# Kernel optimization log

Measured on AMD Instinct MI355X. Metric: run time of the kernel, lower is better.

## Reference

```python
import jax, jax.numpy as jnp
import numpy as np

ALPHA = 0.2  # LeakyReLU negative slope
NEG_INF = -9e15


def _xavier(key, shape, gain=1.414):
    fan_in, fan_out = shape[-2], shape[-1]
    lim = gain * np.sqrt(6.0 / (fan_in + fan_out))
    return jax.random.uniform(key, shape, jnp.float32, -lim, lim)


def setup_inputs() -> dict:
    key = jax.random.key(0)
    ks = jax.random.split(key, 8)
    B, N, Din, H, Dh, Do = 8, 1024, 256, 4, 128, 64
    x = jax.random.normal(ks[0], (B, N, Din), jnp.float32)
    adj = jax.random.randint(ks[1], (B, N, N), 0, 2).astype(jnp.int32)
    W_heads = _xavier(ks[2], (H, Din, Dh))                 # per-head W
    a_heads = _xavier(ks[3], (H, 2 * Dh, 1))[..., 0]       # per-head a, [H, 2*Dh]
    W_out = _xavier(ks[4], (H * Dh, Do))                   # out_att W
    a_out = _xavier(ks[5], (2 * Do, 1))[..., 0]            # out_att a, [2*Do]
    Wf = _xavier(ks[6], (Do, Do), gain=1.0)                # fc_out linear
    bf = jnp.zeros((Do,), jnp.float32)
    return {"x": x, "adj": adj, "W_heads": W_heads, "a_heads": a_heads,
            "W_out": W_out, "a_out": a_out, "Wf": Wf, "bf": bf}


def _leaky_relu(v):
    return jnp.where(v >= 0, v, ALPHA * v)


def _gat(h, adj, W, a):
    # h: [B,N,Fin], adj: [B,N,N], W: [Fin,Fout], a: [2*Fout]
    Wh = h @ W                                   # [B,N,F]
    F = W.shape[-1]
    # additive attention: e_ij = leakyrelu(a_src.Wh_i + a_dst.Wh_j)
    src = Wh @ a[:F]                             # [B,N]
    dst = Wh @ a[F:]                             # [B,N]
    e = _leaky_relu(src[:, :, None] + dst[:, None, :])   # [B,N,N]
    scores = jnp.where(adj > 0, e, NEG_INF)
    attn = jax.nn.softmax(scores, axis=-1)       # dropout is a no-op in eval
    return attn @ Wh                             # [B,N,F]


def reference(x, adj, W_heads, a_heads, W_out, a_out, Wf, bf):
    B, N, _ = x.shape
    H, _, Dh = W_heads.shape
    # multi-head GAT, heads vmapped over leading axis of W_heads / a_heads
    heads = jax.vmap(_gat, in_axes=(None, None, 0, 0))(x, adj, W_heads, a_heads)  # [H,B,N,Dh]
    xcat = jnp.moveaxis(heads, 0, 2).reshape(B, N, H * Dh)   # concat heads, dim=2
    out = jax.nn.elu(_gat(xcat, adj, W_out, a_out))           # [B,N,Do]
    out = jax.nn.relu(out @ Wf + bf)                          # fc_out (dropout no-op)
    return out
```

## Files before the change

### kernel.cpp

```cpp
#include <hip/hip_runtime.h>
#include <hip/hip_bf16.h>

#define BSZ 8
#define NN 1024
#define DIN 256
#define NH 4
#define DH 128
#define DOUT 64
#define RTOT (BSZ*NN)
#define FCAT (NH*DH)
#define ALPHA 0.2f
#define XBLK 1024

typedef unsigned short ushortT;
typedef __attribute__((ext_vector_type(8))) short bf16x8;
typedef __attribute__((ext_vector_type(4))) float f32x4;

static __device__ __forceinline__ ushortT f2bf(float f) {
    __hip_bfloat16 h = __float2bfloat16(f);
    return *reinterpret_cast<ushortT*>(&h);
}
static __device__ __forceinline__ float bfu2f(ushortT u) {
    return __uint_as_float(((unsigned)u) << 16);
}
static __device__ __forceinline__ void split2(float v, ushortT& hi, ushortT& lo) {
    hi = f2bf(v);
    lo = f2bf(v - bfu2f(hi));
}
static __device__ __forceinline__ void gload16(const ushortT* g, ushortT* l) {
    __builtin_amdgcn_global_load_lds(
        (const __attribute__((address_space(1))) unsigned int*)(const void*)g,
        (__attribute__((address_space(3))) unsigned int*)(void*)l, 16, 0, 0);
}

__global__ __launch_bounds__(256) void k_prepw(const float* __restrict__ x,
                                               const float* __restrict__ W,
                                               const float* __restrict__ Wout,
                                               ushortT* __restrict__ xbh, ushortT* __restrict__ xbl,
                                               ushortT* __restrict__ WbTh, ushortT* __restrict__ WbTl,
                                               ushortT* __restrict__ WoTh, ushortT* __restrict__ WoTl) {
    const int bx = blockIdx.x;
    if (bx < XBLK) {
        const int g = bx * 256 + threadIdx.x;
        const float4* p = (const float4*)x + (size_t)g * 2;
        union { ushortT u[8]; uint4 q; } th, tl;
#pragma unroll
        for (int e4 = 0; e4 < 2; ++e4) {
            const float4 v = p[e4];
            split2(v.x, th.u[e4 * 4 + 0], tl.u[e4 * 4 + 0]);
            split2(v.y, th.u[e4 * 4 + 1], tl.u[e4 * 4 + 1]);
            split2(v.z, th.u[e4 * 4 + 2], tl.u[e4 * 4 + 2]);
            split2(v.w, th.u[e4 * 4 + 3], tl.u[e4 * 4 + 3]);
        }
        ((uint4*)xbh)[g] = th.q;
        ((uint4*)xbl)[g] = tl.q;
        return;
    }
    const int g2 = (bx - XBLK) * 256 + threadIdx.x;
    if (g2 < NH * DH * DIN) {
        const int h = g2 >> 15, f = (g2 >> 8) & 127, k = g2 & 255;
        const int kt = k >> 6, k64 = k & 63;
        const float v = W[(size_t)h * DIN * DH + (size_t)k * DH + f];
        ushortT hi, lo; split2(v, hi, lo);
        const int idx = ((h * 4 + kt) * 128 + f) * 64 + k64;
        WbTh[idx] = hi; WbTl[idx] = lo;
    } else {
        const int g3 = g2 - NH * DH * DIN;
        const int f = g3 >> 9, k = g3 & 511;
        const float v = Wout[(size_t)k * DOUT + f];
        ushortT hi, lo; split2(v, hi, lo);
        WoTh[g3] = hi; WoTl[g3] = lo;
    }
}

__global__ __launch_bounds__(512) void k_main(const ushortT* __restrict__ xbh,
                                              const ushortT* __restrict__ xbl,
                                              const float* __restrict__ ah_,
                                              const ushortT* __restrict__ WbTh,
                                              const ushortT* __restrict__ WbTl,
                                              const int* __restrict__ adj,
                                              unsigned* __restrict__ adjbit,
                                              ushortT* __restrict__ WhT,
                                              float* __restrict__ src1,
                                              float* __restrict__ dst1) {
    __shared__ ushortT Ah[128 * 64], Al[128 * 64];
    __shared__ ushortT Bh[128 * 64], Bl[128 * 64];
    __shared__ float sred[8][32], dred[8][32];
    const int tid = threadIdx.x;
    if (blockIdx.x >= 256) {
        const int g = (blockIdx.x - 256) * 512 + tid;
        const int row = g >> 5, w = g & 31;
        const int4* p = (const int4*)(adj + (size_t)row * NN + w * 32);
        unsigned m = 0;
#pragma unroll
        for (int q = 0; q < 8; ++q) {
            const int4 v = p[q];
            m |= (v.x > 0 ? 1u : 0u) << (q * 4 + 0);
            m |= (v.y > 0 ? 1u : 0u) << (q * 4 + 1);
            m |= (v.z > 0 ? 1u : 0u) << (q * 4 + 2);
            m |= (v.w > 0 ? 1u : 0u) << (q * 4 + 3);
        }
        adjbit[g] = m;
        return;
    }
    const int lane = tid & 63, wave = tid >> 6;
    const int h = blockIdx.x >> 6, mt = blockIdx.x & 63;
    const int r0 = mt * 128, b = r0 >> 10, jr = r0 & 1023;
    const int m16 = lane & 15, quad = lane >> 4;
    const int mg = wave >> 1, fg = wave & 1;
    f32x4 acc[2][4];
#pragma unroll
    for (int a = 0; a < 2; ++a)
#pragma unroll
        for (int c = 0; c < 4; ++c) acc[a][c] = (f32x4){0.f, 0.f, 0.f, 0.f};

    for (int kt = 0; kt < 4; ++kt) {
        __syncthreads();
        const ushortT* planeH = WbTh + (size_t)((h * 4 + kt) * 128) * 64;
        const ushortT* planeL = WbTl + (size_t)((h * 4 + kt) * 128) * 64;
#pragma unroll
        for (int half = 0; half < 2; ++half) {
            const int f = wave * 16 + half * 8 + (lane >> 3);
            const int sc = (lane & 7) ^ (f & 7);
            gload16(planeH + (size_t)f * 64 + sc * 8, Bh + (wave * 16 + half * 8) * 64);
            gload16(planeL + (size_t)f * 64 + sc * 8, Bl + (wave * 16 + half * 8) * 64);
        }
#pragma unroll
        for (int half = 0; half < 2; ++half) {
            const int r = wave * 16 + half * 8 + (lane >> 3);
            const int sc = (lane & 7) ^ (r & 7);
            gload16(xbh + (size_t)(r0 + r) * DIN + kt * 64 + sc * 8, Ah + (wave * 16 + half * 8) * 64);
            gload16(xbl + (size_t)(r0 + r) * DIN + kt * 64 + sc * 8, Al + (wave * 16 + half * 8) * 64);
        }
        __syncthreads();
#pragma unroll
        for (int ks = 0; ks < 2; ++ks) {
            bf16x8 a_h[2], a_l[2], b_h[4], b_l[4];
#pragma unroll
            for (int ms = 0; ms < 2; ++ms) {
                const int row = (mg * 2 + ms) * 16 + m16;
                const int cl = (ks * 4 + quad) ^ (row & 7);
                a_h[ms] = *(const bf16x8*)&Ah[row * 64 + cl * 8];
                a_l[ms] = *(const bf16x8*)&Al[row * 64 + cl * 8];
            }
#pragma unroll
            for (int fs = 0; fs < 4; ++fs) {
                const int row = (fg * 4 + fs) * 16 + m16;
                const int cl = (ks * 4 + quad) ^ (row & 7);
                b_h[fs] = *(const bf16x8*)&Bh[row * 64 + cl * 8];
                b_l[fs] = *(const bf16x8*)&Bl[row * 64 + cl * 8];
            }
#pragma unroll
            for (int ms = 0; ms < 2; ++ms)
#pragma unroll
                for (int fs = 0; fs < 4; ++fs) {
                    acc[ms][fs] = __builtin_amdgcn_mfma_f32_16x16x32_bf16(a_h[ms], b_h[fs], acc[ms][fs], 0, 0, 0);
                    acc[ms][fs] = __builtin_amdgcn_mfma_f32_16x16x32_bf16(a_h[ms], b_l[fs], acc[ms][fs], 0, 0, 0);
                    acc[ms][fs] = __builtin_amdgcn_mfma_f32_16x16x32_bf16(a_l[ms], b_h[fs], acc[ms][fs], 0, 0, 0);
                }
        }
    }
    float sacc[2][4] = {{0,0,0,0},{0,0,0,0}}, dacc[2][4] = {{0,0,0,0},{0,0,0,0}};
#pragma unroll
    for (int ms = 0; ms < 2; ++ms)
#pragma unroll
        for (int fs = 0; fs < 4; ++fs) {
            const int fl = (fg * 4 + fs) * 16 + m16;
            const float a_s = ah_[h * 2 * DH + fl];
            const float a_d = ah_[h * 2 * DH + DH + fl];
            union { ushortT u[4]; uint2 q; } tw;
#pragma unroll
            for (int reg = 0; reg < 4; ++reg) {
                const float v = acc[ms][fs][reg];
                sacc[ms][reg] += v * a_s;
                dacc[ms][reg] += v * a_d;
                tw.u[reg] = f2bf(v);
            }
            *(uint2*)(WhT + ((size_t)((b * NH + h) * DH + fl)) * NN + jr + (mg * 2 + ms) * 16 + quad * 4) = tw.q;
        }
#pragma unroll
    for (int ms = 0; ms < 2; ++ms) {
#pragma unroll
        for (int reg = 0; reg < 4; ++reg) {
            float s = sacc[ms][reg], d = dacc[ms][reg];
#pragma unroll
            for (int o = 8; o > 0; o >>= 1) {
                s += __shfl_xor(s, o, 64);
                d += __shfl_xor(d, o, 64);
            }
            if (m16 == 0) {
                sred[wave][ms * 16 + quad * 4 + reg] = s;
                dred[wave][ms * 16 + quad * 4 + reg] = d;
            }
        }
    }
    __syncthreads();
    if (tid < 128) {
        const int mgr = tid >> 5, idx = tid & 31;
        src1[h * RTOT + r0 + tid] = sred[mgr * 2][idx] + sred[mgr * 2 + 1][idx];
        dst1[h * RTOT + r0 + tid] = dred[mgr * 2][idx] + dred[mgr * 2 + 1][idx];
    }
}

__global__ __launch_bounds__(512) void k_attn1(const unsigned* __restrict__ adjbit,
                                               const ushortT* __restrict__ WhT,
                                               const float* __restrict__ src1,
                                               const float* __restrict__ dst1,
                                               ushortT* __restrict__ xcat) {
    __shared__ ushortT As[2][64 * 64];
    __shared__ unsigned maskS[64 * 32];
    __shared__ float dstv[NN];
    __shared__ float srcv[64], rowinv[64], red8[8];
    const int tid = threadIdx.x, lane = tid & 63, wave = tid >> 6;
    const int bh = blockIdx.x & 31, it = blockIdx.x >> 5;
    const int b = bh >> 2, h = bh & 3;
    const int i0 = it * 64;
    const int m16 = lane & 15, quad = lane >> 4;
    const int mg = wave >> 2, fg = wave & 3;

    const unsigned* mbase = adjbit + (size_t)(b * NN + i0) * 32;
#pragma unroll
    for (int k2 = 0; k2 < 4; ++k2) maskS[tid + 512 * k2] = mbase[tid + 512 * k2];
    float lm = -INFINITY;
#pragma unroll
    for (int k2 = 0; k2 < 2; ++k2) {
        const float d = dst1[h * RTOT + b * NN + tid + 512 * k2];
        dstv[tid + 512 * k2] = d;
        lm = fmaxf(lm, d);
    }
    if (tid < 64) srcv[tid] = src1[h * RTOT + b * NN + i0 + tid];
#pragma unroll
    for (int o = 32; o > 0; o >>= 1) lm = fmaxf(lm, __shfl_xor(lm, o, 64));
    if (lane == 0) red8[wave] = lm;
    __syncthreads();
    float dmax = red8[0];
#pragma unroll
    for (int w = 1; w < 8; ++w) dmax = fmaxf(dmax, red8[w]);

    const int arow = tid >> 3, apart = tid & 7;
    const float si = srcv[arow];
    float mrow = si + dmax;
    mrow = mrow >= 0.f ? mrow : ALPHA * mrow;
    float fsum = 0.f;

    const ushortT* Bbase = WhT + (size_t)(bh * DH) * NN;
    f32x4 acc[2][2];
#pragma unroll
    for (int a = 0; a < 2; ++a)
#pragma unroll
        for (int c = 0; c < 2; ++c) acc[a][c] = (f32x4){0.f, 0.f, 0.f, 0.f};

#define STAGE_A(kt_, buf_)                                                                 \
    {                                                                                      \
        const int kt__ = (kt_);                                                            \
        const unsigned w0 = maskS[arow * 32 + kt__ * 2 + (apart >> 2)];                    \
        const int bb = (apart & 3) * 8;                                                    \
        union { ushortT u[8]; uint4 q; } tw;                                               \
        _Pragma("unroll")                                                                  \
        for (int e4 = 0; e4 < 2; ++e4) {                                                   \
            const float4 dv = *(const float4*)&dstv[kt__ * 64 + apart * 8 + e4 * 4];       \
            const float vv[4] = {dv.x, dv.y, dv.z, dv.w};                                  \
            _Pragma("unroll")                                                              \
            for (int e = 0; e < 4; ++e) {                                                  \
                float v = si + vv[e];                                                      \
                v = v >= 0.f ? v : ALPHA * v;                                              \
                const unsigned bit = (w0 >> (bb + e4 * 4 + e)) & 1u;                       \
                const float p = bit ? __expf(v - mrow) : 0.f;                              \
                fsum += p;                                                                 \
                tw.u[e4 * 4 + e] = f2bf(p);                                                \
            }                                                                              \
        }                                                                                  \
        *(uint4*)&As[(buf_)][arow * 64 + (apart ^ (arow & 7)) * 8] = tw.q;                 \
    }
#define LOADB(kt_, dst_)                                                                   \
    {                                                                                      \
        _Pragma("unroll")                                                                  \
        for (int ks = 0; ks < 2; ++ks)                                                     \
            _Pragma("unroll")                                                              \
            for (int ff = 0; ff < 2; ++ff)                                                 \
                dst_[ks][ff] = *(const bf16x8*)(Bbase +                                    \
                    (size_t)(fg * 32 + ff * 16 + m16) * NN + (kt_) * 64 + (ks * 4 + quad) * 8); \
    }
#define MFMA_STEP(buf_, bv_)                                                               \
    {                                                                                      \
        _Pragma("unroll")                                                                  \
        for (int ks = 0; ks < 2; ++ks) {                                                   \
            bf16x8 afr[2];                                                                 \
            _Pragma("unroll")                                                              \
            for (int ms = 0; ms < 2; ++ms) {                                               \
                const int rowa = mg * 32 + ms * 16 + m16;                                  \
                const int cla = (ks * 4 + quad) ^ (rowa & 7);                              \
                afr[ms] = *(const bf16x8*)&As[(buf_)][rowa * 64 + cla * 8];                \
            }                                                                              \
            _Pragma("unroll")                                                              \
            for (int ff = 0; ff < 2; ++ff)                                                 \
                _Pragma("unroll")                                                          \
                for (int ms = 0; ms < 2; ++ms)                                             \
                    acc[ms][ff] = __builtin_amdgcn_mfma_f32_16x16x32_bf16(afr[ms], bv_[ks][ff], acc[ms][ff], 0, 0, 0); \
        }                                                                                  \
    }

    bf16x8 b0v[2][2], b1v[2][2];
    LOADB(0, b0v);
    STAGE_A(0, 0);
    for (int kt = 0; kt < 16; kt += 2) {
        __syncthreads();
        if (kt < 15) { LOADB(kt + 1, b1v); STAGE_A(kt + 1, 1); }
        MFMA_STEP(0, b0v);
        __syncthreads();
        if (kt < 14) { LOADB(kt + 2, b0v); STAGE_A(kt + 2, 0); }
        MFMA_STEP(1, b1v);
    }
#undef STAGE_A
#undef LOADB
#undef MFMA_STEP
#pragma unroll
    for (int o = 1; o < 8; o <<= 1) fsum += __shfl_xor(fsum, o, 64);
    if ((lane & 7) == 0) rowinv[arow] = 1.f / fsum;
    __syncthreads();
#pragma unroll
    for (int ms = 0; ms < 2; ++ms) {
        float rv[4];
#pragma unroll
        for (int reg = 0; reg < 4; ++reg) rv[reg] = rowinv[mg * 32 + ms * 16 + quad * 4 + reg];
#pragma unroll
        for (int ff = 0; ff < 2; ++ff) {
            const int f = h * DH + fg * 32 + ff * 16 + m16;
#pragma unroll
            for (int reg = 0; reg < 4; ++reg) {
                const int i = i0 + mg * 32 + ms * 16 + quad * 4 + reg;
                xcat[(size_t)(b * NN + i) * FCAT + f] = f2bf(acc[ms][ff][reg] * rv[reg]);
            }
        }
    }
}

__global__ __launch_bounds__(256) void k_wh2(const ushortT* __restrict__ xcat,
                                             const ushortT* __restrict__ WoTh,
                                             const ushortT* __restrict__ WoTl,
                                             const float* __restrict__ aout,
                                             ushortT* __restrict__ Wh2T,
                                             float* __restrict__ src2,
                                             float* __restrict__ dst2) {
    __shared__ ushortT As[32 * 64];
    __shared__ ushortT Bh[64 * 64], Bl[64 * 64];
    __shared__ float sred[4][16], dred[4][16];
    const int tid = threadIdx.x, lane = tid & 63, wave = tid >> 6;
    const int r0 = blockIdx.x * 32;
    const int b = r0 >> 10, jr = r0 & 1023;
    const int m16 = lane & 15, quad = lane >> 4;
    const int mg = wave >> 1, fg = wave & 1;
    f32x4 acc[2] = {(f32x4){0.f,0.f,0.f,0.f}, (f32x4){0.f,0.f,0.f,0.f}};

    for (int kt = 0; kt < 8; ++kt) {
        __syncthreads();
        {
            const int row = wave * 8 + (lane >> 3);
            const int sc = (lane & 7) ^ (row & 7);
            gload16(xcat + (size_t)(r0 + row) * FCAT + kt * 64 + sc * 8, As + wave * 8 * 64);
        }
#pragma unroll
        for (int half = 0; half < 2; ++half) {
            const int f = wave * 16 + half * 8 + (lane >> 3);
            const int sc = (lane & 7) ^ (f & 7);
            gload16(WoTh + (size_t)f * FCAT + kt * 64 + sc * 8, Bh + (wave * 16 + half * 8) * 64);
            gload16(WoTl + (size_t)f * FCAT + kt * 64 + sc * 8, Bl + (wave * 16 + half * 8) * 64);
        }
        __syncthreads();
#pragma unroll
        for (int ks = 0; ks < 2; ++ks) {
            const int rowa = mg * 16 + m16;
            const int cla = (ks * 4 + quad) ^ (rowa & 7);
            const bf16x8 afr = *(const bf16x8*)&As[rowa * 64 + cla * 8];
#pragma unroll
            for (int ff = 0; ff < 2; ++ff) {
                const int rowb = fg * 32 + ff * 16 + m16;
                const int clb = (ks * 4 + quad) ^ (rowb & 7);
                const bf16x8 b_h = *(const bf16x8*)&Bh[rowb * 64 + clb * 8];
                const bf16x8 b_l = *(const bf16x8*)&Bl[rowb * 64 + clb * 8];
                acc[ff] = __builtin_amdgcn_mfma_f32_16x16x32_bf16(afr, b_h, acc[ff], 0, 0, 0);
                acc[ff] = __builtin_amdgcn_mfma_f32_16x16x32_bf16(afr, b_l, acc[ff], 0, 0, 0);
            }
        }
    }
    float sv[4] = {0, 0, 0, 0}, dv[4] = {0, 0, 0, 0};
#pragma unroll
    for (int ff = 0; ff < 2; ++ff) {
        const int f = fg * 32 + ff * 16 + m16;
        const float a_s = aout[f], a_d = aout[DOUT + f];
        union { ushortT u[4]; uint2 q; } tw;
#pragma unroll
        for (int reg = 0; reg < 4; ++reg) {
            const float v = acc[ff][reg];
            sv[reg] += v * a_s;
            dv[reg] += v * a_d;
            tw.u[reg] = f2bf(v);
        }
        *(uint2*)(Wh2T + ((size_t)(b * DOUT + f)) * NN + jr + mg * 16 + quad * 4) = tw.q;
    }
#pragma unroll
    for (int reg = 0; reg < 4; ++reg) {
#pragma unroll
        for (int o = 8; o > 0; o >>= 1) {
            sv[reg] += __shfl_xor(sv[reg], o, 64);
            dv[reg] += __shfl_xor(dv[reg], o, 64);
        }
        if (m16 == 0) { sred[wave][quad * 4 + reg] = sv[reg]; dred[wave][quad * 4 + reg] = dv[reg]; }
    }
    __syncthreads();
    if (tid < 32) {
        const int mgr = tid >> 4, idx = tid & 15;
        src2[r0 + tid] = sred[mgr * 2][idx] + sred[mgr * 2 + 1][idx];
        dst2[r0 + tid] = dred[mgr * 2][idx] + dred[mgr * 2 + 1][idx];
    }
}

__global__ __launch_bounds__(512) void k_attn2(const unsigned* __restrict__ adjbit,
                                               const ushortT* __restrict__ Wh2T,
                                               const float* __restrict__ src2,
                                               const float* __restrict__ dst2,
                                               const float* __restrict__ Wf,
                                               const float* __restrict__ bfv,
                                               float* __restrict__ out) {
    __shared__ ushortT As[2][32 * 64];
    __shared__ ushortT Wfh[64 * 64], Wfl[64 * 64];
    __shared__ unsigned maskS[32 * 32];
    __shared__ float dstv[NN];
    __shared__ float t2s[32 * 68];
    __shared__ float srcv[32], rowinv[32], red8[8];
    const int tid = threadIdx.x, lane = tid & 63, wave = tid >> 6;
    const int b = blockIdx.x & 7, it = blockIdx.x >> 3;
    const int i0 = it * 32;
    const int m16 = lane & 15, quad = lane >> 4;

    const unsigned* mbase = adjbit + (size_t)(b * NN + i0) * 32;
#pragma unroll
    for (int k2 = 0; k2 < 2; ++k2) maskS[tid + 512 * k2] = mbase[tid + 512 * k2];
    float lm = -INFINITY;
#pragma unroll
    for (int k2 = 0; k2 < 2; ++k2) {
        const float d = dst2[b * NN + tid + 512 * k2];
        dstv[tid + 512 * k2] = d;
        lm = fmaxf(lm, d);
    }
    if (tid < 32) srcv[tid] = src2[b * NN + i0 + tid];
    {
        const int c = tid & 63, kc = wave * 8;
        union { ushortT u[8]; uint4 q; } th4, tl4;
#pragma unroll
        for (int e = 0; e < 8; ++e)
            split2(Wf[(size_t)(kc + e) * DOUT + c], th4.u[e], tl4.u[e]);
        const int ch = wave ^ (c & 7);
        *(uint4*)&Wfh[c * 64 + ch * 8] = th4.q;
        *(uint4*)&Wfl[c * 64 + ch * 8] = tl4.q;
    }
#pragma unroll
    for (int o = 32; o > 0; o >>= 1) lm = fmaxf(lm, __shfl_xor(lm, o, 64));
    if (lane == 0) red8[wave] = lm;
    __syncthreads();
    float dmax = red8[0];
#pragma unroll
    for (int w = 1; w < 8; ++w) dmax = fmaxf(dmax, red8[w]);

    const int arow = tid >> 4, apart = tid & 15;
    const float si = srcv[arow];
    float mrow = si + dmax;
    mrow = mrow >= 0.f ? mrow : ALPHA * mrow;
    float fsum = 0.f;

    const int mfrag = wave >> 2, fq = wave & 3;
    const ushortT* Bbase = Wh2T + (size_t)(b * DOUT) * NN;
    f32x4 acc4 = (f32x4){0.f, 0.f, 0.f, 0.f};

#define STAGE_A2(kt_, buf_)                                                                \
    {                                                                                      \
        const int kt__ = (kt_);                                                            \
        const unsigned w0 = maskS[arow * 32 + kt__ * 2 + (apart >> 3)];                    \
        const int bb = (apart & 7) * 4;                                                    \
        union { ushortT u[4]; uint2 q; } tw;                                               \
        const float4 dv = *(const float4*)&dstv[kt__ * 64 + apart * 4];                    \
        const float vv[4] = {dv.x, dv.y, dv.z, dv.w};                                      \
        _Pragma("unroll")                                                                  \
        for (int e = 0; e < 4; ++e) {                                                      \
            float v = si + vv[e];                                                          \
            v = v >= 0.f ? v : ALPHA * v;                                                  \
            const unsigned bit = (w0 >> (bb + e)) & 1u;                                    \
            const float p = bit ? __expf(v - mrow) : 0.f;                                  \
            fsum += p;                                                                     \
            tw.u[e] = f2bf(p);                                                             \
        }                                                                                  \
        *(uint2*)&As[(buf_)][arow * 64 + (((apart >> 1) ^ (arow & 7)) * 8) + (apart & 1) * 4] = tw.q; \
    }
#define LOADB2(kt_, dst_)                                                                  \
    {                                                                                      \
        _Pragma("unroll")                                                                  \
        for (int ks = 0; ks < 2; ++ks)                                                     \
            dst_[ks] = *(const bf16x8*)(Bbase +                                            \
                (size_t)(fq * 16 + m16) * NN + (kt_) * 64 + (ks * 4 + quad) * 8);          \
    }
#define MFMA_STEP2(buf_, bv_)                                                              \
    {                                                                                      \
        _Pragma("unroll")                                                                  \
        for (int ks = 0; ks < 2; ++ks) {                                                   \
            const int rowa = mfrag * 16 + m16;                                             \
            const int cla = (ks * 4 + quad) ^ (rowa & 7);                                  \
            const bf16x8 afr = *(const bf16x8*)&As[(buf_)][rowa * 64 + cla * 8];           \
            acc4 = __builtin_amdgcn_mfma_f32_16x16x32_bf16(afr, bv_[ks], acc4, 0, 0, 0);   \
        }                                                                                  \
    }

    bf16x8 b0v[2], b1v[2];
    LOADB2(0, b0v);
    STAGE_A2(0, 0);
    for (int kt = 0; kt < 16; kt += 2) {
        __syncthreads();
        if (kt < 15) { LOADB2(kt + 1, b1v); STAGE_A2(kt + 1, 1); }
        MFMA_STEP2(0, b0v);
        __syncthreads();
        if (kt < 14) { LOADB2(kt + 2, b0v); STAGE_A2(kt + 2, 0); }
        MFMA_STEP2(1, b1v);
    }
#undef STAGE_A2
#undef LOADB2
#undef MFMA_STEP2
#pragma unroll
    for (int o = 1; o < 16; o <<= 1) fsum += __shfl_xor(fsum, o, 64);
    if ((lane & 15) == 0) rowinv[arow] = 1.f / fsum;
    __syncthreads();
#pragma unroll
    for (int reg = 0; reg < 4; ++reg) {
        const int row = mfrag * 16 + quad * 4 + reg;
        float v = acc4[reg] * rowinv[row];
        v = v > 0.f ? v : (__expf(v) - 1.f);
        t2s[row * 68 + fq * 16 + m16] = v;
    }
    __syncthreads();
    const int cc = fq * 16 + m16;
    f32x4 oacc;
    {
        const float bias = bfv[cc];
        oacc = (f32x4){bias, bias, bias, bias};
    }
#pragma unroll
    for (int ks = 0; ks < 2; ++ks) {
        const int rowa = mfrag * 16 + m16;
        const float4 fA = *(const float4*)&t2s[rowa * 68 + ks * 32 + quad * 8];
        const float4 fB = *(const float4*)&t2s[rowa * 68 + ks * 32 + quad * 8 + 4];
        union { ushortT u[8]; bf16x8 v; } a_h, a_l;
        const float av[8] = {fA.x, fA.y, fA.z, fA.w, fB.x, fB.y, fB.z, fB.w};
#pragma unroll
        for (int e = 0; e < 8; ++e) split2(av[e], a_h.u[e], a_l.u[e]);
        const int cl = (ks * 4 + quad) ^ (cc & 7);
        const bf16x8 b_h = *(const bf16x8*)&Wfh[cc * 64 + cl * 8];
        const bf16x8 b_l = *(const bf16x8*)&Wfl[cc * 64 + cl * 8];
        oacc = __builtin_amdgcn_mfma_f32_16x16x32_bf16(a_h.v, b_h, oacc, 0, 0, 0);
        oacc = __builtin_amdgcn_mfma_f32_16x16x32_bf16(a_h.v, b_l, oacc, 0, 0, 0);
        oacc = __builtin_amdgcn_mfma_f32_16x16x32_bf16(a_l.v, b_h, oacc, 0, 0, 0);
    }
#pragma unroll
    for (int reg = 0; reg < 4; ++reg) {
        const int i = i0 + mfrag * 16 + quad * 4 + reg;
        out[(size_t)(b * NN + i) * DOUT + cc] = fmaxf(oacc[reg], 0.f);
    }
}

extern "C" void kernel_launch(void* const* d_in, const int* in_sizes, int n_in,
                              void* d_out, int out_size, void* d_ws, size_t ws_size,
                              hipStream_t stream) {
    const float* x   = (const float*)d_in[0];
    const int*   adj = (const int*)d_in[1];
    const float* Wh  = (const float*)d_in[2];
    const float* ah  = (const float*)d_in[3];
    const float* Wo  = (const float*)d_in[4];
    const float* ao  = (const float*)d_in[5];
    const float* Wf  = (const float*)d_in[6];
    const float* bf  = (const float*)d_in[7];
    float* out = (float*)d_out;

    float* ws    = (float*)d_ws;
    float* src1  = ws;
    float* dst1  = src1 + NH * RTOT;
    float* src2  = dst1 + NH * RTOT;
    float* dst2  = src2 + RTOT;
    ushortT* WhT   = (ushortT*)(dst2 + RTOT);
    ushortT* Wh2T  = WhT + (size_t)RTOT * FCAT;
    ushortT* xcat  = Wh2T + (size_t)RTOT * DOUT;
    ushortT* WbTh  = xcat + (size_t)RTOT * FCAT;
    ushortT* WbTl  = WbTh + NH * DH * DIN;
    ushortT* WoTh  = WbTl + NH * DH * DIN;
    ushortT* WoTl  = WoTh + DOUT * FCAT;
    unsigned* adjbit = (unsigned*)(WoTl + DOUT * FCAT);
    ushortT* xbh  = (ushortT*)(adjbit + (size_t)BSZ * NN * 32);
    ushortT* xbl  = xbh + (size_t)RTOT * DIN;

    hipLaunchKernelGGL(k_prepw, dim3(XBLK + (NH * DH * DIN + DOUT * FCAT) / 256), dim3(256), 0, stream,
                       x, Wh, Wo, xbh, xbl, WbTh, WbTl, WoTh, WoTl);
    hipLaunchKernelGGL(k_main,  dim3(768), dim3(512), 0, stream,
                       xbh, xbl, ah, WbTh, WbTl, adj, adjbit, WhT, src1, dst1);
    hipLaunchKernelGGL(k_attn1, dim3(512), dim3(512), 0, stream,
                       adjbit, WhT, src1, dst1, xcat);
    hipLaunchKernelGGL(k_wh2,   dim3(256), dim3(256), 0, stream,
                       xcat, WoTh, WoTl, ao, Wh2T, src2, dst2);
    hipLaunchKernelGGL(k_attn2, dim3(256), dim3(512), 0, stream,
                       adjbit, Wh2T, src2, dst2, Wf, bf, out);
}
```

Baseline: 156.6 us.

## Restructure attn1: compute attention probabilities in registers, stage Wh in LDS

The first-layer attention kernel now handles 128 query rows per block with 8 waves of 16 rows each. Each wave builds its bf16 probability fragment directly in registers instead of writing it through shared memory. The full 128-feature Wh tile is staged into double-buffered LDS with a gload16 helper and XOR swizzling, so every wave reuses B from LDS across 8 MFMA column tiles. This removes the A-tile LDS round trip and halves the number of redundant B loads from global memory. In exchange it launches half as many blocks, uses more registers and LDS per block, and depends on a gload16 helper defined elsewhere.

```diff
diff --git a/kernel.cpp b/kernel.cpp
--- a/kernel.cpp
+++ b/kernel.cpp
@@ -202,25 +202,42 @@
     }
 }
 
-__global__ __launch_bounds__(512) void k_attn1(const unsigned* __restrict__ adjbit,
-                                               const ushortT* __restrict__ WhT,
-                                               const float* __restrict__ src1,
-                                               const float* __restrict__ dst1,
-                                               ushortT* __restrict__ xcat) {
-    __shared__ ushortT As[2][64 * 64];
-    __shared__ unsigned maskS[64 * 32];
+__global__ __launch_bounds__(512, 2) void k_attn1(const unsigned* __restrict__ adjbit,
+                                                  const ushortT* __restrict__ WhT,
+                                                  const float* __restrict__ src1,
+                                                  const float* __restrict__ dst1,
+                                                  ushortT* __restrict__ xcat) {
+    __shared__ ushortT Bs[2][128 * 64];
+    __shared__ unsigned maskS[128 * 34];
     __shared__ float dstv[NN];
-    __shared__ float srcv[64], rowinv[64], red8[8];
+    __shared__ float rowinv[128], red8[8];
     const int tid = threadIdx.x, lane = tid & 63, wave = tid >> 6;
     const int bh = blockIdx.x & 31, it = blockIdx.x >> 5;
     const int b = bh >> 2, h = bh & 3;
-    const int i0 = it * 64;
+    const int i0 = it * 128;
     const int m16 = lane & 15, quad = lane >> 4;
-    const int mg = wave >> 2, fg = wave & 3;
-
-    const unsigned* mbase = adjbit + (size_t)(b * NN + i0) * 32;
-#pragma unroll
-    for (int k2 = 0; k2 < 4; ++k2) maskS[tid + 512 * k2] = mbase[tid + 512 * k2];
+    const ushortT* Bbase = WhT + (size_t)(bh * DH) * NN;
+
+#define STAGEB(kt_, buf_)                                                                  \
+    {                                                                                      \
+        _Pragma("unroll")                                                                  \
+        for (int half = 0; half < 2; ++half) {                                             \
+            const int f = wave * 16 + half * 8 + (lane >> 3);                              \
+            gload16(Bbase + (size_t)f * NN + (kt_) * 64 + (((lane & 7) ^ (f & 7)) * 8),    \
+                    &Bs[(buf_)][(wave * 16 + half * 8) * 64]);                             \
+        }                                                                                  \
+    }
+
+    STAGEB(0, 0);
+    {
+        const uint4* msrc = (const uint4*)(adjbit + (size_t)(b * NN + i0) * 32) + tid * 2;
+        const uint4 w0 = msrc[0], w1 = msrc[1];
+        unsigned* mdst = &maskS[(tid >> 2) * 34 + (tid & 3) * 8];
+        *(uint2*)&mdst[0] = make_uint2(w0.x, w0.y);
+        *(uint2*)&mdst[2] = make_uint2(w0.z, w0.w);
+        *(uint2*)&mdst[4] = make_uint2(w1.x, w1.y);
+        *(uint2*)&mdst[6] = make_uint2(w1.z, w1.w);
+    }
     float lm = -INFINITY;
 #pragma unroll
     for (int k2 = 0; k2 < 2; ++k2) {
@@ -228,7 +245,7 @@
         dstv[tid + 512 * k2] = d;
         lm = fmaxf(lm, d);
     }
-    if (tid < 64) srcv[tid] = src1[h * RTOT + b * NN + i0 + tid];
+    const float si = src1[h * RTOT + b * NN + i0 + wave * 16 + m16];
 #pragma unroll
     for (int o = 32; o > 0; o >>= 1) lm = fmaxf(lm, __shfl_xor(lm, o, 64));
     if (lane == 0) red8[wave] = lm;
@@ -236,102 +253,67 @@
     float dmax = red8[0];
 #pragma unroll
     for (int w = 1; w < 8; ++w) dmax = fmaxf(dmax, red8[w]);
-
-    const int arow = tid >> 3, apart = tid & 7;
-    const float si = srcv[arow];
     float mrow = si + dmax;
     mrow = mrow >= 0.f ? mrow : ALPHA * mrow;
+
+    f32x4 acc[8];
+#pragma unroll
+    for (int c = 0; c < 8; ++c) acc[c] = (f32x4){0.f, 0.f, 0.f, 0.f};
     float fsum = 0.f;
-
-    const ushortT* Bbase = WhT + (size_t)(bh * DH) * NN;
-    f32x4 acc[2][2];
-#pragma unroll
-    for (int a = 0; a < 2; ++a)
-#pragma unroll
-        for (int c = 0; c < 2; ++c) acc[a][c] = (f32x4){0.f, 0.f, 0.f, 0.f};
-
-#define STAGE_A(kt_, buf_)                                                                 \
-    {                                                                                      \
-        const int kt__ = (kt_);                                                            \
-        const unsigned w0 = maskS[arow * 32 + kt__ * 2 + (apart >> 2)];                    \
-        const int bb = (apart & 3) * 8;                                                    \
-        union { ushortT u[8]; uint4 q; } tw;                                               \
-        _Pragma("unroll")                                                                  \
-        for (int e4 = 0; e4 < 2; ++e4) {                                                   \
-            const float4 dv = *(const float4*)&dstv[kt__ * 64 + apart * 8 + e4 * 4];       \
-            const float vv[4] = {dv.x, dv.y, dv.z, dv.w};                                  \
-            _Pragma("unroll")                                                              \
-            for (int e = 0; e < 4; ++e) {                                                  \
-                float v = si + vv[e];                                                      \
-                v = v >= 0.f ? v : ALPHA * v;                                              \
-                const unsigned bit = (w0 >> (bb + e4 * 4 + e)) & 1u;                       \
-                const float p = bit ? __expf(v - mrow) : 0.f;                              \
-                fsum += p;                                                                 \
-                tw.u[e4 * 4 + e] = f2bf(p);                                                \
-            }                                                                              \
-        }                                                                                  \
-        *(uint4*)&As[(buf_)][arow * 64 + (apart ^ (arow & 7)) * 8] = tw.q;                 \
-    }
-#define LOADB(kt_, dst_)                                                                   \
-    {                                                                                      \
-        _Pragma("unroll")                                                                  \
-        for (int ks = 0; ks < 2; ++ks)                                                     \
-            _Pragma("unroll")                                                              \
-            for (int ff = 0; ff < 2; ++ff)                                                 \
-                dst_[ks][ff] = *(const bf16x8*)(Bbase +                                    \
-                    (size_t)(fg * 32 + ff * 16 + m16) * NN + (kt_) * 64 + (ks * 4 + quad) * 8); \
-    }
-#define MFMA_STEP(buf_, bv_)                                                               \
+    const int arow34 = (wave * 16 + m16) * 34;
+
+#define KSTEP(kt_, buf_)                                                                   \
     {                                                                                      \
         _Pragma("unroll")                                                                  \
         for (int ks = 0; ks < 2; ++ks) {                                                   \
-            bf16x8 afr[2];                                                                 \
+            const unsigned w0 = maskS[arow34 + (kt_) * 2 + ks];                            \
+            const float4 d0 = *(const float4*)&dstv[(kt_) * 64 + ks * 32 + quad * 8];      \
+            const float4 d1 = *(const float4*)&dstv[(kt_) * 64 + ks * 32 + quad * 8 + 4];  \
+            const float dv[8] = {d0.x, d0.y, d0.z, d0.w, d1.x, d1.y, d1.z, d1.w};          \
+            union { ushortT u[8]; bf16x8 v; } pa;                                          \
             _Pragma("unroll")                                                              \
-            for (int ms = 0; ms < 2; ++ms) {                                               \
-                const int rowa = mg * 32 + ms * 16 + m16;                                  \
-                const int cla = (ks * 4 + quad) ^ (rowa & 7);                              \
-                afr[ms] = *(const bf16x8*)&As[(buf_)][rowa * 64 + cla * 8];                \
+            for (int e = 0; e < 8; ++e) {                                                  \
+                float v = si + dv[e];                                                      \
+                v = v >= 0.f ? v : ALPHA * v;                                              \
+                const unsigned bit = (w0 >> (quad * 8 + e)) & 1u;                          \
+                const float p = bit ? __expf(v - mrow) : 0.f;                              \
+                fsum += p;                                                                 \
+                pa.u[e] = f2bf(p);                                                         \
             }                                                                              \
             _Pragma("unroll")                                                              \
-            for (int ff = 0; ff < 2; ++ff)                                                 \
-                _Pragma("unroll")                                                          \
-                for (int ms = 0; ms < 2; ++ms)                                             \
-                    acc[ms][ff] = __builtin_amdgcn_mfma_f32_16x16x32_bf16(afr[ms], bv_[ks][ff], acc[ms][ff], 0, 0, 0); \
+            for (int ff = 0; ff < 8; ++ff) {                                               \
+                const int rowb = ff * 16 + m16;                                            \
+                const bf16x8 bfr = *(const bf16x8*)&Bs[(buf_)][rowb * 64 +                 \
+                    (((ks * 4 + quad) ^ (rowb & 7)) * 8)];                                 \
+                acc[ff] = __builtin_amdgcn_mfma_f32_16x16x32_bf16(pa.v, bfr, acc[ff], 0, 0, 0); \
+            }                                                                              \
         }                                                                                  \
     }
 
-    bf16x8 b0v[2][2], b1v[2][2];
-    LOADB(0, b0v);
-    STAGE_A(0, 0);
     for (int kt = 0; kt < 16; kt += 2) {
-        __syncthreads();
-        if (kt < 15) { LOADB(kt + 1, b1v); STAGE_A(kt + 1, 1); }
-        MFMA_STEP(0, b0v);
-        __syncthreads();
-        if (kt < 14) { LOADB(kt + 2, b0v); STAGE_A(kt + 2, 0); }
-        MFMA_STEP(1, b1v);
-    }
-#undef STAGE_A
-#undef LOADB
-#undef MFMA_STEP
-#pragma unroll
-    for (int o = 1; o < 8; o <<= 1) fsum += __shfl_xor(fsum, o, 64);
-    if ((lane & 7) == 0) rowinv[arow] = 1.f / fsum;
-    __syncthreads();
-#pragma unroll
-    for (int ms = 0; ms < 2; ++ms) {
-        float rv[4];
-#pragma unroll
-        for (int reg = 0; reg < 4; ++reg) rv[reg] = rowinv[mg * 32 + ms * 16 + quad * 4 + reg];
-#pragma unroll
-        for (int ff = 0; ff < 2; ++ff) {
-            const int f = h * DH + fg * 32 + ff * 16 + m16;
-#pragma unroll
-            for (int reg = 0; reg < 4; ++reg) {
-                const int i = i0 + mg * 32 + ms * 16 + quad * 4 + reg;
-                xcat[(size_t)(b * NN + i) * FCAT + f] = f2bf(acc[ms][ff][reg] * rv[reg]);
-            }
-        }
+        if (kt < 15) STAGEB(kt + 1, 1);
+        KSTEP(kt, 0);
+        __syncthreads();
+        if (kt < 14) STAGEB(kt + 2, 0);
+        KSTEP(kt + 1, 1);
+        __syncthreads();
+    }
+#undef STAGEB
+#undef KSTEP
+
+    fsum += __shfl_xor(fsum, 16, 64);
+    fsum += __shfl_xor(fsum, 32, 64);
+    if (quad == 0) rowinv[wave * 16 + m16] = 1.f / fsum;
+    __syncthreads();
+    const float4 rq = *(const float4*)&rowinv[wave * 16 + quad * 4];
+    const float rv[4] = {rq.x, rq.y, rq.z, rq.w};
+#pragma unroll
+    for (int ff = 0; ff < 8; ++ff) {
+        const int f = h * DH + ff * 16 + m16;
+        ushortT* xc = xcat + (size_t)(b * NN + i0 + wave * 16 + quad * 4) * FCAT + f;
+#pragma unroll
+        for (int reg = 0; reg < 4; ++reg)
+            xc[(size_t)reg * FCAT] = f2bf(acc[ff][reg] * rv[reg]);
     }
 }
 
@@ -597,7 +579,7 @@
                        x, Wh, Wo, xbh, xbl, WbTh, WbTl, WoTh, WoTl);
     hipLaunchKernelGGL(k_main,  dim3(768), dim3(512), 0, stream,
                        xbh, xbl, ah, WbTh, WbTl, adj, adjbit, WhT, src1, dst1);
-    hipLaunchKernelGGL(k_attn1, dim3(512), dim3(512), 0, stream,
+    hipLaunchKernelGGL(k_attn1, dim3(256), dim3(512), 0, stream,
                        adjbit, WhT, src1, dst1, xcat);
     hipLaunchKernelGGL(k_wh2,   dim3(256), dim3(256), 0, stream,
                        xcat, WoTh, WoTl, ao, Wh2T, src2, dst2);
```

After: 146.8 us. 6.3% less time.
